# Kernel tuning notes

Measured on AMD Instinct MI355X. Metric: run time of the kernel, lower is better.

The kernel has to match this reference:

```python
import jax, jax.numpy as jnp
import numpy as np
from jax import lax

B, T, I, H = 256, 1024, 64, 128  # batch(padded_length), seq_len, input_size, hidden_size


def setup_inputs() -> dict:
    key = jax.random.key(0)
    k0, k1, k2, k3, k4 = jax.random.split(key, 5)
    s = 1.0 / np.sqrt(H)  # pytorch LSTM default init scale
    return {
        "data": jax.random.normal(k0, (B, T, I), dtype=jnp.float32),
        "W_ih": jax.random.uniform(k1, (4 * H, I), dtype=jnp.float32, minval=-s, maxval=s),
        "W_hh": jax.random.uniform(k2, (4 * H, H), dtype=jnp.float32, minval=-s, maxval=s),
        "b_ih": jax.random.uniform(k3, (4 * H,), dtype=jnp.float32, minval=-s, maxval=s),
        "b_hh": jax.random.uniform(k4, (4 * H,), dtype=jnp.float32, minval=-s, maxval=s),
    }


def reference(data, W_ih, W_hh, b_ih, b_hh):
    # data: [B, T, I]. Original permutes to [T, B, I] and runs a per-timestep
    # single-layer LSTM loop with zero initial state, collecting h_t each step.
    b, t, _ = data.shape
    h_dim = W_hh.shape[1]
    # Precompute input projection for all timesteps: [T, B, 4H]
    xs = jnp.einsum('bti,gi->tbg', data, W_ih) + b_ih + b_hh

    def step(carry, x_t):
        h, c = carry
        gates = x_t + h @ W_hh.T  # [B, 4H]
        i, f, g, o = jnp.split(gates, 4, axis=-1)  # pytorch gate order: i,f,g,o
        i = jax.nn.sigmoid(i)
        f = jax.nn.sigmoid(f)
        g = jnp.tanh(g)
        o = jax.nn.sigmoid(o)
        c = f * c + i * g
        h = o * jnp.tanh(c)
        return (h, c), h

    h0 = jnp.zeros((b, h_dim), dtype=data.dtype)
    _, hs = lax.scan(step, (h0, h0), xs)  # hs: [T, B, H]
    return jnp.transpose(hs, (1, 0, 2))  # [B, T, H]
```

## Files before the change

### kernel.cpp

```cpp
#include <hip/hip_runtime.h>


typedef _Float16 half8  __attribute__((ext_vector_type(8)));
typedef _Float16 half2t __attribute__((ext_vector_type(2)));
typedef float  floatx4  __attribute__((ext_vector_type(4)));

constexpr int Tt = 1024;
constexpr int Ii = 64;
constexpr int Hh = 128;
constexpr int CH = 16;
constexpr int NCH = Tt / CH;

__device__ __forceinline__ float fast_rcp(float x) { return __builtin_amdgcn_rcpf(x); }
__device__ __forceinline__ float exp2_(float x)    { return __builtin_amdgcn_exp2f(x); }
__device__ __forceinline__ half2t pk16(float a, float b) {
    return __builtin_bit_cast(half2t, __builtin_amdgcn_cvt_pkrtz(a, b));
}
#define MFMA16(A, B, C) __builtin_amdgcn_mfma_f32_16x16x32_f16((A), (B), (C), 0, 0, 0)
union H8U { half8 v; half2t p[4]; };

__device__ __forceinline__ half8 cvt8(float4 a, float4 b) {
    H8U u;
    u.p[0] = pk16(a.x, a.y); u.p[1] = pk16(a.z, a.w);
    u.p[2] = pk16(b.x, b.y); u.p[3] = pk16(b.z, b.w);
    return u.v;
}
__device__ __forceinline__ floatx4 splat4(float a) { floatx4 r = {a, a, a, a}; return r; }

__global__ __launch_bounds__(512, 1) void lstm_mfma6(
    const float* __restrict__ data,
    const float* __restrict__ W_ih,
    const float* __restrict__ W_hh,
    const float* __restrict__ b_ih,
    const float* __restrict__ b_hh,
    float* __restrict__ out)
{
    const int b   = blockIdx.x;
    const int t   = threadIdx.x;
    const int w   = t >> 6;
    const int l   = t & 63;
    const int col = l & 15;
    const int kg  = l >> 4;

    half8 bfh[4][4];
    half8 bfx[4][2];
    float bs[4];
#pragma unroll
    for (int g = 0; g < 4; ++g) {
        const float sc = (g == 2) ? -2.8853900817779268f : -1.4426950408889634f;
        const int row = 128 * g + 16 * w + col;
        bs[g] = sc * (b_ih[row] + b_hh[row]);
        const float* wh = W_hh + (size_t)row * Hh;
        const float* wi = W_ih + (size_t)row * Ii;
#pragma unroll
        for (int s = 0; s < 4; ++s) {
            const float* src = wh + 32 * s + 8 * kg;
            const float4 f0 = ((const float4*)src)[0];
            const float4 f1 = ((const float4*)src)[1];
            H8U u;
            u.p[0] = pk16(sc * f0.x, sc * f0.y); u.p[1] = pk16(sc * f0.z, sc * f0.w);
            u.p[2] = pk16(sc * f1.x, sc * f1.y); u.p[3] = pk16(sc * f1.z, sc * f1.w);
            bfh[g][s] = u.v;
        }
#pragma unroll
        for (int s = 0; s < 2; ++s) {
            const float* src = wi + 32 * s + 8 * kg;
            const float4 f0 = ((const float4*)src)[0];
            const float4 f1 = ((const float4*)src)[1];
            H8U u;
            u.p[0] = pk16(sc * f0.x, sc * f0.y); u.p[1] = pk16(sc * f0.z, sc * f0.w);
            u.p[2] = pk16(sc * f1.x, sc * f1.y); u.p[3] = pk16(sc * f1.z, sc * f1.w);
            bfx[g][s] = u.v;
        }
    }

    __shared__ __align__(16) _Float16 hb[2][Hh];

    const float* xp  = data + (size_t)b * Tt * Ii;
    float*       opr = out  + (size_t)b * Tt * Hh + 16 * w + col;

    if (t < Hh) hb[0][t] = (_Float16)0.0f;

    const float* xbase = xp + (size_t)(l & 15) * Ii + 8 * kg;
    float4 xf0 = *(const float4*)(xbase);
    float4 xf1 = *(const float4*)(xbase + 4);
    float4 xf2 = *(const float4*)(xbase + 32);
    float4 xf3 = *(const float4*)(xbase + 36);

    half8 ax0 = cvt8(xf0, xf1);
    half8 ax1 = cvt8(xf2, xf3);
    xf0 = *(const float4*)(xbase + CH * Ii);
    xf1 = *(const float4*)(xbase + CH * Ii + 4);
    xf2 = *(const float4*)(xbase + CH * Ii + 32);
    xf3 = *(const float4*)(xbase + CH * Ii + 36);
    floatx4 xw0 = MFMA16(ax0, bfx[0][0], splat4(bs[0]));
    floatx4 xw1 = MFMA16(ax0, bfx[1][0], splat4(bs[1]));
    floatx4 xw2 = MFMA16(ax0, bfx[2][0], splat4(bs[2]));
    floatx4 xw3 = MFMA16(ax0, bfx[3][0], splat4(bs[3]));
    xw0 = MFMA16(ax1, bfx[0][1], xw0);
    xw1 = MFMA16(ax1, bfx[1][1], xw1);
    xw2 = MFMA16(ax1, bfx[2][1], xw2);
    xw3 = MFMA16(ax1, bfx[3][1], xw3);

    half8 nax0, nax1;
    floatx4 nxw0, nxw1, nxw2, nxw3;

    float c = 0.0f;
    __syncthreads();

#pragma unroll 1
    for (int n = 0; n < NCH; ++n) {
        const float* xb2 = xbase + (size_t)((n + 2 < NCH) ? n + 2 : NCH - 1) * CH * Ii;

#define STEP(P, R, CUR, XTRA)                                                 \
        {                                                                     \
            const _Float16* hbase = &hb[CUR][8 * kg];                         \
            const half8 ah0 = *(const half8*)(hbase);                         \
            const half8 ah1 = *(const half8*)(hbase + 32);                    \
            const half8 ah2 = *(const half8*)(hbase + 64);                    \
            const half8 ah3 = *(const half8*)(hbase + 96);                    \
            XTRA;                                                             \
            __builtin_amdgcn_s_setprio(1);                                    \
            floatx4 qf = MFMA16(ah0, bfh[1][0], xw1);                 \
            floatx4 qg = MFMA16(ah0, bfh[2][0], xw2);                 \
            floatx4 qi = MFMA16(ah0, bfh[0][0], xw0);                 \
            qf = MFMA16(ah1, bfh[1][1], qf);                                  \
            qg = MFMA16(ah1, bfh[2][1], qg);                                  \
            qi = MFMA16(ah1, bfh[0][1], qi);                                  \
            floatx4 qo = MFMA16(ah0, bfh[3][0], xw3);                 \
            qf = MFMA16(ah2, bfh[1][2], qf);                                  \
            qg = MFMA16(ah2, bfh[2][2], qg);                                  \
            qi = MFMA16(ah2, bfh[0][2], qi);                                  \
            qo = MFMA16(ah1, bfh[3][1], qo);                                  \
            qf = MFMA16(ah3, bfh[1][3], qf);                                  \
            qg = MFMA16(ah3, bfh[2][3], qg);                                  \
            qi = MFMA16(ah3, bfh[0][3], qi);                                  \
            qo = MFMA16(ah2, bfh[3][2], qo);                                  \
            const float fg = fast_rcp(1.0f + exp2_(qf[R]));                   \
            const float eg = exp2_(qg[R]);                                    \
            const float fc = fg * c;                                          \
            const float gv = (1.0f - eg) * fast_rcp(1.0f + eg);               \
            const float ig = fast_rcp(1.0f + exp2_(qi[R]));                   \
            c = fmaf(ig, gv, fc);                                             \
            const float ec = exp2_(-2.8853900817779268f * c);                 \
            const float tc = (1.0f - ec) * fast_rcp(1.0f + ec);               \
            qo = MFMA16(ah3, bfh[3][3], qo);                                  \
            __builtin_amdgcn_s_setprio(0);                                    \
            const float og = fast_rcp(1.0f + exp2_(qo[R]));                   \
            const float h  = og * tc;                                         \
            if (kg == (P)) {                                                  \
                hb[(CUR) ^ 1][16 * w + col] = (_Float16)h;                    \
                *opr = h;                                                     \
            }                                                                 \
            opr += Hh;                                                        \
            asm volatile("s_waitcnt lgkmcnt(0)\n\ts_barrier" ::: "memory");   \
        }

#define PHASE(P, X0, X1, X2, X3)                                              \
        STEP(P, 0, 0, X0) STEP(P, 1, 1, X1) STEP(P, 2, 0, X2) STEP(P, 3, 1, X3)

        PHASE(0,
              (c = __shfl(c, (l + 48) & 63), nax0 = cvt8(xf0, xf1)),
              nax1 = cvt8(xf2, xf3),
              nxw0 = MFMA16(nax0, bfx[0][0], splat4(bs[0])),
              nxw1 = MFMA16(nax0, bfx[1][0], splat4(bs[1])))
        PHASE(1,
              (c = __shfl(c, (l + 48) & 63), nxw2 = MFMA16(nax0, bfx[2][0], splat4(bs[2]))),
              nxw3 = MFMA16(nax0, bfx[3][0], splat4(bs[3])),
              nxw0 = MFMA16(nax1, bfx[0][1], nxw0),
              nxw1 = MFMA16(nax1, bfx[1][1], nxw1))
        PHASE(2,
              (c = __shfl(c, (l + 48) & 63), nxw2 = MFMA16(nax1, bfx[2][1], nxw2)),
              nxw3 = MFMA16(nax1, bfx[3][1], nxw3),
              xf0 = *(const float4*)(xb2),
              xf1 = *(const float4*)(xb2 + 4))
        PHASE(3,
              (c = __shfl(c, (l + 48) & 63), xf2 = *(const float4*)(xb2 + 32)),
              xf3 = *(const float4*)(xb2 + 36),
              (void)0,
              (void)0)
#undef PHASE
#undef STEP

        xw0 = nxw0; xw1 = nxw1; xw2 = nxw2; xw3 = nxw3;
    }
}

extern "C" void kernel_launch(void* const* d_in, const int* in_sizes, int n_in,
                              void* d_out, int out_size, void* d_ws, size_t ws_size,
                              hipStream_t stream) {
    const float* data = (const float*)d_in[0];
    const float* W_ih = (const float*)d_in[1];
    const float* W_hh = (const float*)d_in[2];
    const float* b_ih = (const float*)d_in[3];
    const float* b_hh = (const float*)d_in[4];
    float* out = (float*)d_out;

    hipLaunchKernelGGL(lstm_mfma6, dim3(256), dim3(512), 0, stream,
                       data, W_ih, W_hh, b_ih, b_hh, out);
}
```

Baseline: 416.8 us.

## Quantize recurrent h and W_hh to int8 and use i8 MFMA

Replaces the fp16 recurrent matmul with int8 MFMA (16x16x64). W_hh is quantized per gate with a row-max scale and h is quantized as h*127, which halves the MFMA count on the serial per-step critical path and shrinks the shared-memory h buffer. The dequantized result is folded into the sigmoid/tanh arguments with an fma against the precomputed input projection. This trades noticeable accuracy for fewer recurrent-step instructions, and int8 error on h accumulated over 1024 steps may exceed the tolerance.

```diff
diff --git a/kernel.cpp b/kernel.cpp
--- a/kernel.cpp
+++ b/kernel.cpp
@@ -4,6 +4,7 @@
 typedef _Float16 half8  __attribute__((ext_vector_type(8)));
 typedef _Float16 half2t __attribute__((ext_vector_type(2)));
 typedef float  floatx4  __attribute__((ext_vector_type(4)));
+typedef int    intx4   __attribute__((ext_vector_type(4)));
 
 constexpr int Tt = 1024;
 constexpr int Ii = 64;
@@ -17,7 +18,9 @@
     return __builtin_bit_cast(half2t, __builtin_amdgcn_cvt_pkrtz(a, b));
 }
 #define MFMA16(A, B, C) __builtin_amdgcn_mfma_f32_16x16x32_f16((A), (B), (C), 0, 0, 0)
+#define MFMAI8(A, B, C) __builtin_amdgcn_mfma_i32_16x16x64_i8((A), (B), (C), 0, 0, 0)
 union H8U { half8 v; half2t p[4]; };
+union I8U { intx4 v; signed char c[16]; };
 
 __device__ __forceinline__ half8 cvt8(float4 a, float4 b) {
     H8U u;
@@ -27,7 +30,7 @@
 }
 __device__ __forceinline__ floatx4 splat4(float a) { floatx4 r = {a, a, a, a}; return r; }
 
-__global__ __launch_bounds__(512, 1) void lstm_mfma6(
+__global__ __launch_bounds__(512, 1) void lstm_mfma7(
     const float* __restrict__ data,
     const float* __restrict__ W_ih,
     const float* __restrict__ W_hh,
@@ -42,7 +45,8 @@
     const int col = l & 15;
     const int kg  = l >> 4;
 
-    half8 bfh[4][4];
+    intx4 bqh[4][2];
+    float dqh[4];
     half8 bfx[4][2];
     float bs[4];
 #pragma unroll
@@ -52,15 +56,23 @@
         bs[g] = sc * (b_ih[row] + b_hh[row]);
         const float* wh = W_hh + (size_t)row * Hh;
         const float* wi = W_ih + (size_t)row * Ii;
-#pragma unroll
-        for (int s = 0; s < 4; ++s) {
-            const float* src = wh + 32 * s + 8 * kg;
-            const float4 f0 = ((const float4*)src)[0];
-            const float4 f1 = ((const float4*)src)[1];
-            H8U u;
-            u.p[0] = pk16(sc * f0.x, sc * f0.y); u.p[1] = pk16(sc * f0.z, sc * f0.w);
-            u.p[2] = pk16(sc * f1.x, sc * f1.y); u.p[3] = pk16(sc * f1.z, sc * f1.w);
-            bfh[g][s] = u.v;
+        float mw = 1e-20f;
+#pragma unroll
+        for (int k = 0; k < Hh; k += 4) {
+            const float4 f = *(const float4*)(wh + k);
+            mw = fmaxf(mw, fmaxf(fmaxf(fabsf(f.x), fabsf(f.y)),
+                                 fmaxf(fabsf(f.z), fabsf(f.w))));
+        }
+        const float qs = 127.f / mw;
+        dqh[g] = sc * mw * (1.f / (127.f * 127.f));
+#pragma unroll
+        for (int s = 0; s < 2; ++s) {
+            const float* src = wh + 64 * s + 16 * kg;
+            I8U u;
+#pragma unroll
+            for (int j = 0; j < 16; ++j)
+                u.c[j] = (signed char)(int)rintf(src[j] * qs);
+            bqh[g][s] = u.v;
         }
 #pragma unroll
         for (int s = 0; s < 2; ++s) {
@@ -74,12 +86,12 @@
         }
     }
 
-    __shared__ __align__(16) _Float16 hb[2][Hh];
+    __shared__ __align__(16) signed char hbq[2][Hh];
 
     const float* xp  = data + (size_t)b * Tt * Ii;
     float*       opr = out  + (size_t)b * Tt * Hh + 16 * w + col;
 
-    if (t < Hh) hb[0][t] = (_Float16)0.0f;
+    if (t < Hh) hbq[0][t] = 0;
 
     const float* xbase = xp + (size_t)(l & 15) * Ii + 8 * kg;
     float4 xf0 = *(const float4*)(xbase);
@@ -114,42 +126,34 @@
 
 #define STEP(P, R, CUR, XTRA)                                                 \
         {                                                                     \
-            const _Float16* hbase = &hb[CUR][8 * kg];                         \
-            const half8 ah0 = *(const half8*)(hbase);                         \
-            const half8 ah1 = *(const half8*)(hbase + 32);                    \
-            const half8 ah2 = *(const half8*)(hbase + 64);                    \
-            const half8 ah3 = *(const half8*)(hbase + 96);                    \
+            const signed char* hbase = &hbq[CUR][16 * kg];                    \
+            const intx4 ah0 = *(const intx4*)(hbase);                         \
+            const intx4 ah1 = *(const intx4*)(hbase + 64);                    \
             XTRA;                                                             \
             __builtin_amdgcn_s_setprio(1);                                    \
-            floatx4 qf = MFMA16(ah0, bfh[1][0], xw1);                 \
-            floatx4 qg = MFMA16(ah0, bfh[2][0], xw2);                 \
-            floatx4 qi = MFMA16(ah0, bfh[0][0], xw0);                 \
-            qf = MFMA16(ah1, bfh[1][1], qf);                                  \
-            qg = MFMA16(ah1, bfh[2][1], qg);                                  \
-            qi = MFMA16(ah1, bfh[0][1], qi);                                  \
-            floatx4 qo = MFMA16(ah0, bfh[3][0], xw3);                 \
-            qf = MFMA16(ah2, bfh[1][2], qf);                                  \
-            qg = MFMA16(ah2, bfh[2][2], qg);                                  \
-            qi = MFMA16(ah2, bfh[0][2], qi);                                  \
-            qo = MFMA16(ah1, bfh[3][1], qo);                                  \
-            qf = MFMA16(ah3, bfh[1][3], qf);                                  \
-            qg = MFMA16(ah3, bfh[2][3], qg);                                  \
-            qi = MFMA16(ah3, bfh[0][3], qi);                                  \
-            qo = MFMA16(ah2, bfh[3][2], qo);                                  \
-            const float fg = fast_rcp(1.0f + exp2_(qf[R]));                   \
-            const float eg = exp2_(qg[R]);                                    \
+            const intx4 z4 = {0, 0, 0, 0};                                    \
+            intx4 qf = MFMAI8(ah0, bqh[1][0], z4);                     \
+            intx4 qg = MFMAI8(ah0, bqh[2][0], z4);                     \
+            intx4 qi = MFMAI8(ah0, bqh[0][0], z4);                     \
+            qf = MFMAI8(ah1, bqh[1][1], qf);                                  \
+            qg = MFMAI8(ah1, bqh[2][1], qg);                                  \
+            qi = MFMAI8(ah1, bqh[0][1], qi);                                  \
+            intx4 qo = MFMAI8(ah0, bqh[3][0], z4);                     \
+            const float fg = fast_rcp(1.0f + exp2_(fmaf((float)qf[R], dqh[1], xw1[R]))); \
+            const float eg = exp2_(fmaf((float)qg[R], dqh[2], xw2[R]));       \
+            qo = MFMAI8(ah1, bqh[3][1], qo);                                  \
             const float fc = fg * c;                                          \
             const float gv = (1.0f - eg) * fast_rcp(1.0f + eg);               \
-            const float ig = fast_rcp(1.0f + exp2_(qi[R]));                   \
+            const float ig = fast_rcp(1.0f + exp2_(fmaf((float)qi[R], dqh[0], xw0[R]))); \
+            __builtin_amdgcn_s_setprio(0);                                    \
             c = fmaf(ig, gv, fc);                                             \
             const float ec = exp2_(-2.8853900817779268f * c);                 \
             const float tc = (1.0f - ec) * fast_rcp(1.0f + ec);               \
-            qo = MFMA16(ah3, bfh[3][3], qo);                                  \
-            __builtin_amdgcn_s_setprio(0);                                    \
-            const float og = fast_rcp(1.0f + exp2_(qo[R]));                   \
+            const float og = fast_rcp(1.0f + exp2_(fmaf((float)qo[R], dqh[3], xw3[R]))); \
             const float h  = og * tc;                                         \
             if (kg == (P)) {                                                  \
-                hb[(CUR) ^ 1][16 * w + col] = (_Float16)h;                    \
+                hbq[(CUR) ^ 1][16 * w + col] =                                \
+                    (signed char)(int)rintf(h * 127.f);                       \
                 *opr = h;                                                     \
             }                                                                 \
             opr += Hh;                                                        \
@@ -196,6 +200,6 @@
     const float* b_hh = (const float*)d_in[4];
     float* out = (float*)d_out;
 
-    hipLaunchKernelGGL(lstm_mfma6, dim3(256), dim3(512), 0, stream,
+    hipLaunchKernelGGL(lstm_mfma7, dim3(256), dim3(512), 0, stream,
                        data, W_ih, W_hh, b_ih, b_hh, out);
 }
```

New measurement: 489.4 us. 17.4% more time.

## Halve workgroup to 4 waves, each computing two 16-column hidden tiles

Applied to the files above, without the earlier changes.

Each block now runs 256 threads (4 waves) instead of 512, and each wave handles 32 hidden units as two independent 16-column tiles. The per-step weight fragments, gate MFMAs and cell states are doubled per wave and interleaved. The aim is to cut the per-step barrier cost across fewer waves and give each wave two independent dependency chains to overlap MFMA latency with the activation math. The cost is twice the registers for weights and more serial MFMA work per wave on the critical path. The s_setprio hints are dropped.

```diff
diff --git a/kernel.cpp b/kernel.cpp
--- a/kernel.cpp
+++ b/kernel.cpp
@@ -27,7 +27,9 @@
 }
 __device__ __forceinline__ floatx4 splat4(float a) { floatx4 r = {a, a, a, a}; return r; }
 
-__global__ __launch_bounds__(512, 1) void lstm_mfma6(
+__global__
+__attribute__((amdgpu_flat_work_group_size(256, 256), amdgpu_waves_per_eu(1, 1)))
+void lstm_w4(
     const float* __restrict__ data,
     const float* __restrict__ W_ih,
     const float* __restrict__ W_hh,
@@ -42,44 +44,46 @@
     const int col = l & 15;
     const int kg  = l >> 4;
 
-    half8 bfh[4][4];
-    half8 bfx[4][2];
-    float bs[4];
+    half8 bfh[4][2][4];
+    half8 bfx[4][2][2];
+    float bs[4][2];
 #pragma unroll
     for (int g = 0; g < 4; ++g) {
         const float sc = (g == 2) ? -2.8853900817779268f : -1.4426950408889634f;
-        const int row = 128 * g + 16 * w + col;
-        bs[g] = sc * (b_ih[row] + b_hh[row]);
-        const float* wh = W_hh + (size_t)row * Hh;
-        const float* wi = W_ih + (size_t)row * Ii;
-#pragma unroll
-        for (int s = 0; s < 4; ++s) {
-            const float* src = wh + 32 * s + 8 * kg;
-            const float4 f0 = ((const float4*)src)[0];
-            const float4 f1 = ((const float4*)src)[1];
-            H8U u;
-            u.p[0] = pk16(sc * f0.x, sc * f0.y); u.p[1] = pk16(sc * f0.z, sc * f0.w);
-            u.p[2] = pk16(sc * f1.x, sc * f1.y); u.p[3] = pk16(sc * f1.z, sc * f1.w);
-            bfh[g][s] = u.v;
-        }
-#pragma unroll
-        for (int s = 0; s < 2; ++s) {
-            const float* src = wi + 32 * s + 8 * kg;
-            const float4 f0 = ((const float4*)src)[0];
-            const float4 f1 = ((const float4*)src)[1];
-            H8U u;
-            u.p[0] = pk16(sc * f0.x, sc * f0.y); u.p[1] = pk16(sc * f0.z, sc * f0.w);
-            u.p[2] = pk16(sc * f1.x, sc * f1.y); u.p[3] = pk16(sc * f1.z, sc * f1.w);
-            bfx[g][s] = u.v;
+#pragma unroll
+        for (int tau = 0; tau < 2; ++tau) {
+            const int row = 128 * g + 32 * w + 16 * tau + col;
+            bs[g][tau] = sc * (b_ih[row] + b_hh[row]);
+            const float* wh = W_hh + (size_t)row * Hh;
+            const float* wi = W_ih + (size_t)row * Ii;
+#pragma unroll
+            for (int s = 0; s < 4; ++s) {
+                const float* src = wh + 32 * s + 8 * kg;
+                const float4 f0 = ((const float4*)src)[0];
+                const float4 f1 = ((const float4*)src)[1];
+                H8U u;
+                u.p[0] = pk16(sc * f0.x, sc * f0.y); u.p[1] = pk16(sc * f0.z, sc * f0.w);
+                u.p[2] = pk16(sc * f1.x, sc * f1.y); u.p[3] = pk16(sc * f1.z, sc * f1.w);
+                bfh[g][tau][s] = u.v;
+            }
+#pragma unroll
+            for (int s = 0; s < 2; ++s) {
+                const float* src = wi + 32 * s + 8 * kg;
+                const float4 f0 = ((const float4*)src)[0];
+                const float4 f1 = ((const float4*)src)[1];
+                H8U u;
+                u.p[0] = pk16(sc * f0.x, sc * f0.y); u.p[1] = pk16(sc * f0.z, sc * f0.w);
+                u.p[2] = pk16(sc * f1.x, sc * f1.y); u.p[3] = pk16(sc * f1.z, sc * f1.w);
+                bfx[g][tau][s] = u.v;
+            }
         }
     }
 
     __shared__ __align__(16) _Float16 hb[2][Hh];
+    if (t < Hh) hb[0][t] = (_Float16)0.0f;
 
     const float* xp  = data + (size_t)b * Tt * Ii;
-    float*       opr = out  + (size_t)b * Tt * Hh + 16 * w + col;
-
-    if (t < Hh) hb[0][t] = (_Float16)0.0f;
+    float*       opr = out  + (size_t)b * Tt * Hh + 32 * w + col;
 
     const float* xbase = xp + (size_t)(l & 15) * Ii + 8 * kg;
     float4 xf0 = *(const float4*)(xbase);
@@ -93,19 +97,27 @@
     xf1 = *(const float4*)(xbase + CH * Ii + 4);
     xf2 = *(const float4*)(xbase + CH * Ii + 32);
     xf3 = *(const float4*)(xbase + CH * Ii + 36);
-    floatx4 xw0 = MFMA16(ax0, bfx[0][0], splat4(bs[0]));
-    floatx4 xw1 = MFMA16(ax0, bfx[1][0], splat4(bs[1]));
-    floatx4 xw2 = MFMA16(ax0, bfx[2][0], splat4(bs[2]));
-    floatx4 xw3 = MFMA16(ax0, bfx[3][0], splat4(bs[3]));
-    xw0 = MFMA16(ax1, bfx[0][1], xw0);
-    xw1 = MFMA16(ax1, bfx[1][1], xw1);
-    xw2 = MFMA16(ax1, bfx[2][1], xw2);
-    xw3 = MFMA16(ax1, bfx[3][1], xw3);
+    floatx4 xw_i0 = MFMA16(ax0, bfx[0][0][0], splat4(bs[0][0]));
+    floatx4 xw_f0 = MFMA16(ax0, bfx[1][0][0], splat4(bs[1][0]));
+    floatx4 xw_g0 = MFMA16(ax0, bfx[2][0][0], splat4(bs[2][0]));
+    floatx4 xw_o0 = MFMA16(ax0, bfx[3][0][0], splat4(bs[3][0]));
+    floatx4 xw_i1 = MFMA16(ax0, bfx[0][1][0], splat4(bs[0][1]));
+    floatx4 xw_f1 = MFMA16(ax0, bfx[1][1][0], splat4(bs[1][1]));
+    floatx4 xw_g1 = MFMA16(ax0, bfx[2][1][0], splat4(bs[2][1]));
+    floatx4 xw_o1 = MFMA16(ax0, bfx[3][1][0], splat4(bs[3][1]));
+    xw_i0 = MFMA16(ax1, bfx[0][0][1], xw_i0);
+    xw_f0 = MFMA16(ax1, bfx[1][0][1], xw_f0);
+    xw_g0 = MFMA16(ax1, bfx[2][0][1], xw_g0);
+    xw_o0 = MFMA16(ax1, bfx[3][0][1], xw_o0);
+    xw_i1 = MFMA16(ax1, bfx[0][1][1], xw_i1);
+    xw_f1 = MFMA16(ax1, bfx[1][1][1], xw_f1);
+    xw_g1 = MFMA16(ax1, bfx[2][1][1], xw_g1);
+    xw_o1 = MFMA16(ax1, bfx[3][1][1], xw_o1);
 
     half8 nax0, nax1;
-    floatx4 nxw0, nxw1, nxw2, nxw3;
-
-    float c = 0.0f;
+    floatx4 nxw_i0, nxw_f0, nxw_g0, nxw_o0, nxw_i1, nxw_f1, nxw_g1, nxw_o1;
+
+    float c0 = 0.0f, c1 = 0.0f;
     __syncthreads();
 
 #pragma unroll 1
@@ -120,37 +132,63 @@
             const half8 ah2 = *(const half8*)(hbase + 64);                    \
             const half8 ah3 = *(const half8*)(hbase + 96);                    \
             XTRA;                                                             \
-            __builtin_amdgcn_s_setprio(1);                                    \
-            floatx4 qf = MFMA16(ah0, bfh[1][0], xw1);                 \
-            floatx4 qg = MFMA16(ah0, bfh[2][0], xw2);                 \
-            floatx4 qi = MFMA16(ah0, bfh[0][0], xw0);                 \
-            qf = MFMA16(ah1, bfh[1][1], qf);                                  \
-            qg = MFMA16(ah1, bfh[2][1], qg);                                  \
-            qi = MFMA16(ah1, bfh[0][1], qi);                                  \
-            floatx4 qo = MFMA16(ah0, bfh[3][0], xw3);                 \
-            qf = MFMA16(ah2, bfh[1][2], qf);                                  \
-            qg = MFMA16(ah2, bfh[2][2], qg);                                  \
-            qi = MFMA16(ah2, bfh[0][2], qi);                                  \
-            qo = MFMA16(ah1, bfh[3][1], qo);                                  \
-            qf = MFMA16(ah3, bfh[1][3], qf);                                  \
-            qg = MFMA16(ah3, bfh[2][3], qg);                                  \
-            qi = MFMA16(ah3, bfh[0][3], qi);                                  \
-            qo = MFMA16(ah2, bfh[3][2], qo);                                  \
-            const float fg = fast_rcp(1.0f + exp2_(qf[R]));                   \
-            const float eg = exp2_(qg[R]);                                    \
-            const float fc = fg * c;                                          \
-            const float gv = (1.0f - eg) * fast_rcp(1.0f + eg);               \
-            const float ig = fast_rcp(1.0f + exp2_(qi[R]));                   \
-            c = fmaf(ig, gv, fc);                                             \
-            const float ec = exp2_(-2.8853900817779268f * c);                 \
-            const float tc = (1.0f - ec) * fast_rcp(1.0f + ec);               \
-            qo = MFMA16(ah3, bfh[3][3], qo);                                  \
-            __builtin_amdgcn_s_setprio(0);                                    \
-            const float og = fast_rcp(1.0f + exp2_(qo[R]));                   \
-            const float h  = og * tc;                                         \
+            floatx4 qf0 = MFMA16(ah0, bfh[1][0][0], xw_f0);                   \
+            floatx4 qg0 = MFMA16(ah0, bfh[2][0][0], xw_g0);                   \
+            floatx4 qf1 = MFMA16(ah0, bfh[1][1][0], xw_f1);                   \
+            floatx4 qg1 = MFMA16(ah0, bfh[2][1][0], xw_g1);                   \
+            qf0 = MFMA16(ah1, bfh[1][0][1], qf0);                             \
+            qg0 = MFMA16(ah1, bfh[2][0][1], qg0);                             \
+            qf1 = MFMA16(ah1, bfh[1][1][1], qf1);                             \
+            qg1 = MFMA16(ah1, bfh[2][1][1], qg1);                             \
+            floatx4 qi0 = MFMA16(ah0, bfh[0][0][0], xw_i0);                   \
+            floatx4 qi1 = MFMA16(ah0, bfh[0][1][0], xw_i1);                   \
+            qf0 = MFMA16(ah2, bfh[1][0][2], qf0);                             \
+            qg0 = MFMA16(ah2, bfh[2][0][2], qg0);                             \
+            qf1 = MFMA16(ah2, bfh[1][1][2], qf1);                             \
+            qg1 = MFMA16(ah2, bfh[2][1][2], qg1);                             \
+            qi0 = MFMA16(ah1, bfh[0][0][1], qi0);                             \
+            qi1 = MFMA16(ah1, bfh[0][1][1], qi1);                             \
+            qf0 = MFMA16(ah3, bfh[1][0][3], qf0);                             \
+            qg0 = MFMA16(ah3, bfh[2][0][3], qg0);                             \
+            qf1 = MFMA16(ah3, bfh[1][1][3], qf1);                             \
+            qg1 = MFMA16(ah3, bfh[2][1][3], qg1);                             \
+            floatx4 qo0 = MFMA16(ah0, bfh[3][0][0], xw_o0);                   \
+            floatx4 qo1 = MFMA16(ah0, bfh[3][1][0], xw_o1);                   \
+            qi0 = MFMA16(ah2, bfh[0][0][2], qi0);                             \
+            qi1 = MFMA16(ah2, bfh[0][1][2], qi1);                             \
+            const float fg0 = fast_rcp(1.0f + exp2_(qf0[R]));                 \
+            const float eg0 = exp2_(qg0[R]);                                  \
+            const float fg1 = fast_rcp(1.0f + exp2_(qf1[R]));                 \
+            const float eg1 = exp2_(qg1[R]);                                  \
+            qo0 = MFMA16(ah1, bfh[3][0][1], qo0);                             \
+            qo1 = MFMA16(ah1, bfh[3][1][1], qo1);                             \
+            const float fc0 = fg0 * c0;                                       \
+            const float gv0 = (1.0f - eg0) * fast_rcp(1.0f + eg0);            \
+            const float fc1 = fg1 * c1;                                       \
+            const float gv1 = (1.0f - eg1) * fast_rcp(1.0f + eg1);            \
+            qi0 = MFMA16(ah3, bfh[0][0][3], qi0);                             \
+            qi1 = MFMA16(ah3, bfh[0][1][3], qi1);                             \
+            qo0 = MFMA16(ah2, bfh[3][0][2], qo0);                             \
+            qo1 = MFMA16(ah2, bfh[3][1][2], qo1);                             \
+            const float ig0 = fast_rcp(1.0f + exp2_(qi0[R]));                 \
+            const float ig1 = fast_rcp(1.0f + exp2_(qi1[R]));                 \
+            c0 = fmaf(ig0, gv0, fc0);                                         \
+            c1 = fmaf(ig1, gv1, fc1);                                         \
+            qo0 = MFMA16(ah3, bfh[3][0][3], qo0);                             \
+            qo1 = MFMA16(ah3, bfh[3][1][3], qo1);                             \
+            const float ec0 = exp2_(-2.8853900817779268f * c0);               \
+            const float ec1 = exp2_(-2.8853900817779268f * c1);               \
+            const float tc0 = (1.0f - ec0) * fast_rcp(1.0f + ec0);            \
+            const float tc1 = (1.0f - ec1) * fast_rcp(1.0f + ec1);            \
+            const float og0 = fast_rcp(1.0f + exp2_(qo0[R]));                 \
+            const float og1 = fast_rcp(1.0f + exp2_(qo1[R]));                 \
+            const float h0 = og0 * tc0;                                       \
+            const float h1 = og1 * tc1;                                       \
             if (kg == (P)) {                                                  \
-                hb[(CUR) ^ 1][16 * w + col] = (_Float16)h;                    \
-                *opr = h;                                                     \
+                hb[(CUR) ^ 1][32 * w + col]      = (_Float16)h0;              \
+                hb[(CUR) ^ 1][32 * w + 16 + col] = (_Float16)h1;              \
+                *opr       = h0;                                              \
+                *(opr + 16) = h1;                                             \
             }                                                                 \
             opr += Hh;                                                        \
             asm volatile("s_waitcnt lgkmcnt(0)\n\ts_barrier" ::: "memory");   \
@@ -160,29 +198,42 @@
         STEP(P, 0, 0, X0) STEP(P, 1, 1, X1) STEP(P, 2, 0, X2) STEP(P, 3, 1, X3)
 
         PHASE(0,
-              (c = __shfl(c, (l + 48) & 63), nax0 = cvt8(xf0, xf1)),
+              (c0 = __shfl(c0, (l + 48) & 63), c1 = __shfl(c1, (l + 48) & 63),
+               nax0 = cvt8(xf0, xf1)),
               nax1 = cvt8(xf2, xf3),
-              nxw0 = MFMA16(nax0, bfx[0][0], splat4(bs[0])),
-              nxw1 = MFMA16(nax0, bfx[1][0], splat4(bs[1])))
+              (nxw_i0 = MFMA16(nax0, bfx[0][0][0], splat4(bs[0][0])),
+               nxw_i1 = MFMA16(nax0, bfx[0][1][0], splat4(bs[0][1]))),
+              (nxw_f0 = MFMA16(nax0, bfx[1][0][0], splat4(bs[1][0])),
+               nxw_f1 = MFMA16(nax0, bfx[1][1][0], splat4(bs[1][1]))))
         PHASE(1,
-              (c = __shfl(c, (l + 48) & 63), nxw2 = MFMA16(nax0, bfx[2][0], splat4(bs[2]))),
-              nxw3 = MFMA16(nax0, bfx[3][0], splat4(bs[3])),
-              nxw0 = MFMA16(nax1, bfx[0][1], nxw0),
-              nxw1 = MFMA16(nax1, bfx[1][1], nxw1))
+              (c0 = __shfl(c0, (l + 48) & 63), c1 = __shfl(c1, (l + 48) & 63),
+               nxw_g0 = MFMA16(nax0, bfx[2][0][0], splat4(bs[2][0]))),
+              (nxw_g1 = MFMA16(nax0, bfx[2][1][0], splat4(bs[2][1])),
+               nxw_o0 = MFMA16(nax0, bfx[3][0][0], splat4(bs[3][0]))),
+              (nxw_o1 = MFMA16(nax0, bfx[3][1][0], splat4(bs[3][1])),
+               nxw_i0 = MFMA16(nax1, bfx[0][0][1], nxw_i0)),
+              (nxw_i1 = MFMA16(nax1, bfx[0][1][1], nxw_i1),
+               nxw_f0 = MFMA16(nax1, bfx[1][0][1], nxw_f0)))
         PHASE(2,
-              (c = __shfl(c, (l + 48) & 63), nxw2 = MFMA16(nax1, bfx[2][1], nxw2)),
-              nxw3 = MFMA16(nax1, bfx[3][1], nxw3),
-              xf0 = *(const float4*)(xb2),
-              xf1 = *(const float4*)(xb2 + 4))
+              (c0 = __shfl(c0, (l + 48) & 63), c1 = __shfl(c1, (l + 48) & 63),
+               nxw_f1 = MFMA16(nax1, bfx[1][1][1], nxw_f1)),
+              (nxw_g0 = MFMA16(nax1, bfx[2][0][1], nxw_g0),
+               nxw_g1 = MFMA16(nax1, bfx[2][1][1], nxw_g1)),
+              (nxw_o0 = MFMA16(nax1, bfx[3][0][1], nxw_o0),
+               nxw_o1 = MFMA16(nax1, bfx[3][1][1], nxw_o1)),
+              (xf0 = *(const float4*)(xb2),
+               xf1 = *(const float4*)(xb2 + 4)))
         PHASE(3,
-              (c = __shfl(c, (l + 48) & 63), xf2 = *(const float4*)(xb2 + 32)),
+              (c0 = __shfl(c0, (l + 48) & 63), c1 = __shfl(c1, (l + 48) & 63),
+               xf2 = *(const float4*)(xb2 + 32)),
               xf3 = *(const float4*)(xb2 + 36),
               (void)0,
               (void)0)
 #undef PHASE
 #undef STEP
 
-        xw0 = nxw0; xw1 = nxw1; xw2 = nxw2; xw3 = nxw3;
+        xw_i0 = nxw_i0; xw_f0 = nxw_f0; xw_g0 = nxw_g0; xw_o0 = nxw_o0;
+        xw_i1 = nxw_i1; xw_f1 = nxw_f1; xw_g1 = nxw_g1; xw_o1 = nxw_o1;
     }
 }
 
@@ -196,6 +247,6 @@
     const float* b_hh = (const float*)d_in[4];
     float* out = (float*)d_out;
 
-    hipLaunchKernelGGL(lstm_mfma6, dim3(256), dim3(512), 0, stream,
+    hipLaunchKernelGGL(lstm_w4, dim3(256), dim3(256), 0, stream,
                        data, W_ih, W_hh, b_ih, b_hh, out);
 }
```

Result: slower. 475.7 us (+14.1%).
